# Performance work log

Measured on AMD Instinct MI355X. Metric: run time of the kernel, lower is better.

## Reference

```python
import jax, jax.numpy as jnp
import numpy as np

B, C, L = 64, 64, 8192
EPS = float(np.finfo(np.float32).eps)  # matches np.finfo(np.float32).eps in the torch code


def setup_inputs() -> dict:
    key = jax.random.key(0)
    k1, k2, k3 = jax.random.split(key, 3)
    data = jax.random.normal(k1, (B, C, L), dtype=jnp.float32)
    idxes = jax.random.randint(k2, (B, L), 0, L).astype(jnp.int32)
    # prefix lengths in [1, L] so every slice is non-empty (ragged branch)
    zero_pos = jax.random.randint(k3, (B,), 1, L + 1)
    return {"data": data, "idxes": idxes, "zero_pos": zero_pos}


def reference(data, idxes, zero_pos):
    # data: [B, C, L]; per-batch mean/std over the prefix data[b, :, :zero_pos[b]]
    Bn, Cn, Ln = data.shape
    mask = (jnp.arange(Ln)[None, :] < zero_pos[:, None])[:, None, :].astype(data.dtype)  # [B,1,L]
    cnt = Cn * zero_pos.astype(data.dtype)  # [B] number of elements in each prefix
    mean = jnp.sum(data * mask, axis=(1, 2)) / cnt  # [B]
    diff = (data - mean[:, None, None]) * mask  # [B,C,L]
    var = jnp.sum(diff * diff, axis=(1, 2)) / (cnt - 1.0)  # unbiased, as torch.std
    std = jnp.sqrt(var)  # [B]
    out = (data - mean[:, None, None]) / (std[:, None, None] + EPS)
    return (out, idxes, zero_pos)
```

## Files before the change

### kernel.cpp

```cpp
#include <hip/hip_runtime.h>
#include <math.h>

#define BB 64
#define CC 64
#define LL 8192
#define EPS_F 1.1920928955078125e-07f
#define SPLITS 32

#define NORM_BLOCKS_PER_B 64
#define NB_NORM (BB * NORM_BLOCKS_PER_B)
#define NB_AUX  512

typedef float f4 __attribute__((ext_vector_type(4)));
typedef int   i4 __attribute__((ext_vector_type(4)));


__global__ __launch_bounds__(256) void tln_stats(const float* __restrict__ data,
                          const int* __restrict__ zero_pos,
                          float2* __restrict__ partials) {
    const int b = blockIdx.x;
    const int s = blockIdx.y;
    const int tid = threadIdx.x;
    const int zp = zero_pos[b];
    const int nv = zp >> 2;
    const float* base = data + (size_t)b * CC * LL;
    const float* row0 = base + (size_t)s * LL;
    const float* row1 = base + (size_t)(s + SPLITS) * LL;
    const f4* p0 = (const f4*)row0;
    const f4* p1 = (const f4*)row1;

    float s0 = 0.f, s1 = 0.f, s2 = 0.f, s3 = 0.f;
    float q0 = 0.f, q1 = 0.f, q2 = 0.f, q3 = 0.f;
    int i = tid;
    for (; i + 256 < nv; i += 512) {
        f4 a = p0[i], c = p0[i + 256], d = p1[i], e = p1[i + 256];
        s0 += a.x+a.y+a.z+a.w;  q0 += a.x*a.x+a.y*a.y+a.z*a.z+a.w*a.w;
        s1 += c.x+c.y+c.z+c.w;  q1 += c.x*c.x+c.y*c.y+c.z*c.z+c.w*c.w;
        s2 += d.x+d.y+d.z+d.w;  q2 += d.x*d.x+d.y*d.y+d.z*d.z+d.w*d.w;
        s3 += e.x+e.y+e.z+e.w;  q3 += e.x*e.x+e.y*e.y+e.z*e.z+e.w*e.w;
    }
    for (; i < nv; i += 256) {
        f4 a = p0[i], d = p1[i];
        s0 += a.x+a.y+a.z+a.w;  q0 += a.x*a.x+a.y*a.y+a.z*a.z+a.w*a.w;
        s2 += d.x+d.y+d.z+d.w;  q2 += d.x*d.x+d.y*d.y+d.z*d.z+d.w*d.w;
    }
    for (int l = (nv << 2) + tid; l < zp; l += 256) {
        float v0 = row0[l], v1 = row1[l];
        s0 += v0; q0 += v0 * v0;
        s2 += v1; q2 += v1 * v1;
    }
    float sum = (s0 + s1) + (s2 + s3);
    float sq  = (q0 + q1) + (q2 + q3);

    #pragma unroll
    for (int off = 32; off > 0; off >>= 1) {
        sum += __shfl_down(sum, off);
        sq  += __shfl_down(sq, off);
    }
    __shared__ float lsum[4], lsq[4];
    const int wave = tid >> 6;
    const int lane = tid & 63;
    if (lane == 0) { lsum[wave] = sum; lsq[wave] = sq; }
    __syncthreads();
    if (tid == 0) {
        float2 p;
        p.x = lsum[0] + lsum[1] + lsum[2] + lsum[3];
        p.y = lsq[0] + lsq[1] + lsq[2] + lsq[3];
        partials[b * SPLITS + s] = p;
    }
}

__global__ __launch_bounds__(256) void tln_fused(const f4* __restrict__ data4,
                          const float2* __restrict__ partials,
                          const int* __restrict__ zero_pos,
                          const i4* __restrict__ idxes,
                          f4* __restrict__ out4,
                          f4* __restrict__ out_idx,
                          float* __restrict__ out_zp) {
    const int blk = blockIdx.x;
    const int tid = threadIdx.x;

    if (blk < NB_NORM) {
        const int b = blk >> 6;
        const int t = blk & 63;
        const int lane = tid & 63;

        float2 p = partials[(b << 5) + (lane & 31)];
        float s_ = p.x, q_ = p.y;
        #pragma unroll
        for (int off = 16; off > 0; off >>= 1) {
            s_ += __shfl_xor(s_, off);
            q_ += __shfl_xor(q_, off);
        }
        const float cnt  = (float)CC * (float)zero_pos[b];
        const float mean = s_ / cnt;
        const float var  = (q_ - cnt * mean * mean) / (cnt - 1.0f);
        const float inv  = 1.0f / (sqrtf(var) + EPS_F);

        const size_t base = ((size_t)b << 17) | ((size_t)t << 11) | (size_t)tid;
        f4 cur = data4[base];
        #pragma unroll
        for (int k = 0; k < 7; ++k) {
            f4 nxt = data4[base + (size_t)((k + 1) << 8)];
            __builtin_nontemporal_store((cur - mean) * inv,
                                        out4 + base + (size_t)(k << 8));
            cur = nxt;
        }
        __builtin_nontemporal_store((cur - mean) * inv, out4 + base + (size_t)(7 << 8));
    } else {
        const int j = blk - NB_NORM;
        const int i = j * 256 + tid;
        i4 v = idxes[i];
        f4 o = __builtin_convertvector(v, f4);
        __builtin_nontemporal_store(o, out_idx + i);
        if (j == 0 && tid < BB) out_zp[tid] = (float)zero_pos[tid];
    }
}

extern "C" void kernel_launch(void* const* d_in, const int* in_sizes, int n_in,
                              void* d_out, int out_size, void* d_ws, size_t ws_size,
                              hipStream_t stream) {
    const float* data    = (const float*)d_in[0];
    const int* idxes     = (const int*)d_in[1];
    const int* zero_pos  = (const int*)d_in[2];

    float2* partials = (float2*)d_ws;

    float* out_data = (float*)d_out;
    float* out_idx  = out_data + (size_t)BB * CC * LL;
    float* out_zp   = out_idx + (size_t)BB * LL;

    tln_stats<<<dim3(BB, SPLITS), 256, 0, stream>>>(data, zero_pos, partials);

    tln_fused<<<NB_NORM + NB_AUX, 256, 0, stream>>>(
        (const f4*)data, partials, zero_pos, (const i4*)idxes,
        (f4*)out_data, (f4*)out_idx, out_zp);
}
```

Baseline: 244.7 us.

## Split stats into per-row blocks, move idx conversion to stats kernel, halve norm tiles

The stats kernel now runs one block per (batch, channel) row, 4096 blocks instead of 2048, with a 4-way unrolled vector loop. The index-to-float conversion and zero_pos copy move from the normalize kernel into the stats kernel. The normalize kernel now uses 8192 blocks, each handling 4 vectors per thread instead of 8, and reduces 64 partials per batch. The aim is more parallelism and better load balance across the ragged prefixes, with the auxiliary work running alongside the lighter stats pass. The cost is more, smaller blocks and a slightly larger partial reduction.

```diff
diff --git a/kernel.cpp b/kernel.cpp
--- a/kernel.cpp
+++ b/kernel.cpp
@@ -5,11 +5,12 @@
 #define CC 64
 #define LL 8192
 #define EPS_F 1.1920928955078125e-07f
-#define SPLITS 32
 
-#define NORM_BLOCKS_PER_B 64
-#define NB_NORM (BB * NORM_BLOCKS_PER_B)
+#define NB_STAT (BB * CC)
 #define NB_AUX  512
+#define ROW4 (LL / 4)
+
+#define NB_NORM 8192
 
 typedef float f4 __attribute__((ext_vector_type(4)));
 typedef int   i4 __attribute__((ext_vector_type(4)));
@@ -17,104 +18,103 @@
 
 __global__ __launch_bounds__(256) void tln_stats(const float* __restrict__ data,
                           const int* __restrict__ zero_pos,
-                          float2* __restrict__ partials) {
-    const int b = blockIdx.x;
-    const int s = blockIdx.y;
+                          const i4* __restrict__ idxes,
+                          float2* __restrict__ partials,
+                          f4* __restrict__ out_idx,
+                          float* __restrict__ out_zp) {
+    const int blk = blockIdx.x;
     const int tid = threadIdx.x;
-    const int zp = zero_pos[b];
-    const int nv = zp >> 2;
-    const float* base = data + (size_t)b * CC * LL;
-    const float* row0 = base + (size_t)s * LL;
-    const float* row1 = base + (size_t)(s + SPLITS) * LL;
-    const f4* p0 = (const f4*)row0;
-    const f4* p1 = (const f4*)row1;
 
-    float s0 = 0.f, s1 = 0.f, s2 = 0.f, s3 = 0.f;
-    float q0 = 0.f, q1 = 0.f, q2 = 0.f, q3 = 0.f;
-    int i = tid;
-    for (; i + 256 < nv; i += 512) {
-        f4 a = p0[i], c = p0[i + 256], d = p1[i], e = p1[i + 256];
-        s0 += a.x+a.y+a.z+a.w;  q0 += a.x*a.x+a.y*a.y+a.z*a.z+a.w*a.w;
-        s1 += c.x+c.y+c.z+c.w;  q1 += c.x*c.x+c.y*c.y+c.z*c.z+c.w*c.w;
-        s2 += d.x+d.y+d.z+d.w;  q2 += d.x*d.x+d.y*d.y+d.z*d.z+d.w*d.w;
-        s3 += e.x+e.y+e.z+e.w;  q3 += e.x*e.x+e.y*e.y+e.z*e.z+e.w*e.w;
-    }
-    for (; i < nv; i += 256) {
-        f4 a = p0[i], d = p1[i];
-        s0 += a.x+a.y+a.z+a.w;  q0 += a.x*a.x+a.y*a.y+a.z*a.z+a.w*a.w;
-        s2 += d.x+d.y+d.z+d.w;  q2 += d.x*d.x+d.y*d.y+d.z*d.z+d.w*d.w;
-    }
-    for (int l = (nv << 2) + tid; l < zp; l += 256) {
-        float v0 = row0[l], v1 = row1[l];
-        s0 += v0; q0 += v0 * v0;
-        s2 += v1; q2 += v1 * v1;
-    }
-    float sum = (s0 + s1) + (s2 + s3);
-    float sq  = (q0 + q1) + (q2 + q3);
+    if (blk < NB_STAT) {
+        const int b = blk >> 6;
+        const int c = blk & 63;
+        const int zp = zero_pos[b];
+        const int nv = zp >> 2;
+        const float* rowp = data + ((size_t)b * CC + c) * LL;
+        const f4* p = (const f4*)rowp;
 
-    #pragma unroll
-    for (int off = 32; off > 0; off >>= 1) {
-        sum += __shfl_down(sum, off);
-        sq  += __shfl_down(sq, off);
-    }
-    __shared__ float lsum[4], lsq[4];
-    const int wave = tid >> 6;
-    const int lane = tid & 63;
-    if (lane == 0) { lsum[wave] = sum; lsq[wave] = sq; }
-    __syncthreads();
-    if (tid == 0) {
-        float2 p;
-        p.x = lsum[0] + lsum[1] + lsum[2] + lsum[3];
-        p.y = lsq[0] + lsq[1] + lsq[2] + lsq[3];
-        partials[b * SPLITS + s] = p;
+        float s0 = 0.f, s1 = 0.f, s2 = 0.f, s3 = 0.f;
+        float q0 = 0.f, q1 = 0.f, q2 = 0.f, q3 = 0.f;
+        int i = tid;
+        for (; i + 768 < nv; i += 1024) {
+            f4 a = p[i], d = p[i + 256], e = p[i + 512], g = p[i + 768];
+            s0 += a.x+a.y+a.z+a.w;  q0 += a.x*a.x+a.y*a.y+a.z*a.z+a.w*a.w;
+            s1 += d.x+d.y+d.z+d.w;  q1 += d.x*d.x+d.y*d.y+d.z*d.z+d.w*d.w;
+            s2 += e.x+e.y+e.z+e.w;  q2 += e.x*e.x+e.y*e.y+e.z*e.z+e.w*e.w;
+            s3 += g.x+g.y+g.z+g.w;  q3 += g.x*g.x+g.y*g.y+g.z*g.z+g.w*g.w;
+        }
+        for (; i < nv; i += 256) {
+            f4 a = p[i];
+            s0 += a.x+a.y+a.z+a.w;  q0 += a.x*a.x+a.y*a.y+a.z*a.z+a.w*a.w;
+        }
+        {
+            const int l = (nv << 2) + tid;
+            if (l < zp) {
+                float v = rowp[l];
+                s0 += v; q0 += v * v;
+            }
+        }
+        float sum = (s0 + s1) + (s2 + s3);
+        float sq  = (q0 + q1) + (q2 + q3);
+
+        #pragma unroll
+        for (int off = 32; off > 0; off >>= 1) {
+            sum += __shfl_down(sum, off);
+            sq  += __shfl_down(sq, off);
+        }
+        __shared__ float lsum[4], lsq[4];
+        const int wave = tid >> 6;
+        const int lane = tid & 63;
+        if (lane == 0) { lsum[wave] = sum; lsq[wave] = sq; }
+        __syncthreads();
+        if (tid == 0) {
+            float2 pr;
+            pr.x = lsum[0] + lsum[1] + lsum[2] + lsum[3];
+            pr.y = lsq[0] + lsq[1] + lsq[2] + lsq[3];
+            partials[blk] = pr;
+        }
+    } else {
+        const int j = blk - NB_STAT;
+        const int ii = j * 256 + tid;
+        i4 v = idxes[ii];
+        f4 o = __builtin_convertvector(v, f4);
+        __builtin_nontemporal_store(o, out_idx + ii);
+        if (j == 0 && tid < BB) out_zp[tid] = (float)zero_pos[tid];
     }
 }
 
 __global__ __launch_bounds__(256) void tln_fused(const f4* __restrict__ data4,
                           const float2* __restrict__ partials,
                           const int* __restrict__ zero_pos,
-                          const i4* __restrict__ idxes,
-                          f4* __restrict__ out4,
-                          f4* __restrict__ out_idx,
-                          float* __restrict__ out_zp) {
+                          f4* __restrict__ out4) {
     const int blk = blockIdx.x;
     const int tid = threadIdx.x;
+    const int b = blk >> 7;
+    const int t = blk & 127;
+    const int lane = tid & 63;
 
-    if (blk < NB_NORM) {
-        const int b = blk >> 6;
-        const int t = blk & 63;
-        const int lane = tid & 63;
+    float2 p = partials[(b << 6) + lane];
+    float s_ = p.x, q_ = p.y;
+    #pragma unroll
+    for (int off = 32; off > 0; off >>= 1) {
+        s_ += __shfl_xor(s_, off);
+        q_ += __shfl_xor(q_, off);
+    }
+    const float cnt  = (float)CC * (float)zero_pos[b];
+    const float mean = s_ / cnt;
+    const float var  = (q_ - cnt * mean * mean) / (cnt - 1.0f);
+    const float inv  = 1.0f / (sqrtf(var) + EPS_F);
 
-        float2 p = partials[(b << 5) + (lane & 31)];
-        float s_ = p.x, q_ = p.y;
-        #pragma unroll
-        for (int off = 16; off > 0; off >>= 1) {
-            s_ += __shfl_xor(s_, off);
-            q_ += __shfl_xor(q_, off);
-        }
-        const float cnt  = (float)CC * (float)zero_pos[b];
-        const float mean = s_ / cnt;
-        const float var  = (q_ - cnt * mean * mean) / (cnt - 1.0f);
-        const float inv  = 1.0f / (sqrtf(var) + EPS_F);
-
-        const size_t base = ((size_t)b << 17) | ((size_t)t << 11) | (size_t)tid;
-        f4 cur = data4[base];
-        #pragma unroll
-        for (int k = 0; k < 7; ++k) {
-            f4 nxt = data4[base + (size_t)((k + 1) << 8)];
-            __builtin_nontemporal_store((cur - mean) * inv,
-                                        out4 + base + (size_t)(k << 8));
-            cur = nxt;
-        }
-        __builtin_nontemporal_store((cur - mean) * inv, out4 + base + (size_t)(7 << 8));
-    } else {
-        const int j = blk - NB_NORM;
-        const int i = j * 256 + tid;
-        i4 v = idxes[i];
-        f4 o = __builtin_convertvector(v, f4);
-        __builtin_nontemporal_store(o, out_idx + i);
-        if (j == 0 && tid < BB) out_zp[tid] = (float)zero_pos[tid];
+    const size_t base = ((size_t)b << 17) | ((size_t)t << 10) | (size_t)tid;
+    f4 cur = data4[base];
+    #pragma unroll
+    for (int k = 0; k < 3; ++k) {
+        f4 nxt = data4[base + (size_t)((k + 1) << 8)];
+        __builtin_nontemporal_store((cur - mean) * inv,
+                                    out4 + base + (size_t)(k << 8));
+        cur = nxt;
     }
+    __builtin_nontemporal_store((cur - mean) * inv, out4 + base + (size_t)(3 << 8));
 }
 
 extern "C" void kernel_launch(void* const* d_in, const int* in_sizes, int n_in,
@@ -130,9 +130,9 @@
     float* out_idx  = out_data + (size_t)BB * CC * LL;
     float* out_zp   = out_idx + (size_t)BB * LL;
 
-    tln_stats<<<dim3(BB, SPLITS), 256, 0, stream>>>(data, zero_pos, partials);
+    tln_stats<<<NB_STAT + NB_AUX, 256, 0, stream>>>(
+        data, zero_pos, (const i4*)idxes, partials, (f4*)out_idx, out_zp);
 
-    tln_fused<<<NB_NORM + NB_AUX, 256, 0, stream>>>(
-        (const f4*)data, partials, zero_pos, (const i4*)idxes,
-        (f4*)out_data, (f4*)out_idx, out_zp);
+    tln_fused<<<NB_NORM, 256, 0, stream>>>(
+        (const f4*)data, partials, zero_pos, (f4*)out_data);
 }
```

Result: no change. 241.4 us (-1.3%).
